# Optimization experiments

Hardware: AMD Instinct MI355X
Metric: run time of the kernel (lower is better)

## Reference

```python
import jax, jax.numpy as jnp
import numpy as np
import math

FIRE_THRESH = 0.85
SQRT_2_OVER_PI = math.sqrt(2.0 / math.pi)

def _gelu(x):
    # tanh-approx GELU, exactly as in the torch module
    return 0.5 * x * (1.0 + jnp.tanh(SQRT_2_OVER_PI * (x + 0.044715 * x * x * x)))

def setup_inputs() -> dict:
    key = jax.random.key(0)
    ks = jax.random.split(key, 8)
    B, T, D, N = 8, 4096, 1024, 512
    x = jax.random.normal(ks[0], (B, T, D), dtype=jnp.float32)
    log_beta = jnp.asarray(math.log(10.0), dtype=jnp.float32)
    log_k_inject = jnp.asarray(math.log(0.1), dtype=jnp.float32)
    # buffer keys are stored L2-normalized in the original module
    raw_keys = jax.random.normal(ks[1], (N, D), dtype=jnp.float32)
    buf_keys = raw_keys / jnp.maximum(jnp.linalg.norm(raw_keys, axis=-1, keepdims=True), 1e-12)
    buf_vals = jax.random.normal(ks[2], (N, D), dtype=jnp.float32)
    global_sum = jax.random.normal(ks[3], (D,), dtype=jnp.float32)
    mask = jnp.ones((N,), dtype=bool)
    hit_count = jax.random.randint(ks[4], (N,), 0, 100, dtype=jnp.int64 if jax.config.jax_enable_x64 else jnp.int32)
    n_global = 300
    return {"x": x, "log_beta": log_beta, "log_k_inject": log_k_inject,
            "buf_keys": buf_keys, "buf_vals": buf_vals, "global_sum": global_sum,
            "mask": mask, "hit_count": hit_count, "n_global": n_global}

def reference(x, log_beta, log_k_inject, buf_keys, buf_vals, global_sum, mask, hit_count, n_global):
    B, T, D = x.shape
    y = _gelu(x)  # [B,T,D]
    # m_curr = mean over all tokens, detached in the original
    m_curr = jax.lax.stop_gradient(jnp.mean(y.reshape(-1, D), axis=0))  # [D]
    beta = jnp.clip(jnp.exp(log_beta), 1.0, 50.0)
    k_inject = jnp.clip(jnp.exp(log_k_inject), 0.001, 2.0)
    # retrieval (no_grad block in torch)
    q = m_curr / jnp.maximum(jnp.linalg.norm(m_curr), 1e-12)  # [D]
    sims = buf_keys @ q                                        # [N]
    logits = jnp.where(mask, beta * sims, -1e9)
    attn = jax.nn.softmax(logits, axis=0)
    retrieved = attn @ buf_vals                                # [D]
    nearest_idx = jnp.argmax(logits)
    sims_plain = jnp.where(mask, sims, -1.0)
    hit = hit_count[nearest_idx] + (sims_plain[nearest_idx] > FIRE_THRESH).astype(hit_count.dtype)
    t = k_inject * jnp.log(hit.astype(x.dtype) + 1.0)
    global_mean = global_sum / max(int(n_global), 1)
    delta = jax.lax.stop_gradient(retrieved - global_mean)     # [D]
    return y + t * delta.reshape(1, 1, D)
```

## Files before the change

### kernel.cpp

```cpp
#include <hip/hip_runtime.h>
#include <math.h>

#define ROWS 32768
#define D    1024
#define DF4  256
#define NKEYS 512

__device__ __forceinline__ float gelu1(float x) {
    float z = 0.7978845608028654f * fmaf(0.044715f * x, x * x, x);
    float e = __expf(2.0f * z);
    return x - x / (e + 1.0f);
}

__global__ __launch_bounds__(256) void k_colsum(const float4* __restrict__ x4,
                                                float4* __restrict__ partial) {
    int t = threadIdx.x;
    int b = blockIdx.x;
    const float4* p = x4 + (size_t)b * 64 * DF4 + t;
    float4 acc = make_float4(0.f, 0.f, 0.f, 0.f);
#pragma unroll 8
    for (int r = 0; r < 64; ++r) {
        float4 v = p[(size_t)r * DF4];
        acc.x += gelu1(v.x);
        acc.y += gelu1(v.y);
        acc.z += gelu1(v.z);
        acc.w += gelu1(v.w);
    }
    partial[b * DF4 + t] = acc;
}

__global__ __launch_bounds__(1024) void k_red1(const float* __restrict__ partial,
                                               float* __restrict__ partial2) {
    int d = threadIdx.x;
    int b = blockIdx.x;
    float s = 0.f;
#pragma unroll
    for (int p = 0; p < 32; ++p) s += partial[(size_t)(b * 32 + p) * D + d];
    partial2[b * D + d] = s;
}

__global__ __launch_bounds__(1024) void k_q(const float* __restrict__ partial2,
                                            float* __restrict__ q) {
    __shared__ float red[1024];
    int d = threadIdx.x;
    float s = 0.f;
#pragma unroll
    for (int p = 0; p < 16; ++p) s += partial2[p * D + d];
    float m = s * (1.0f / 32768.0f);
    red[d] = m * m;
    __syncthreads();
    for (int st = 512; st > 0; st >>= 1) {
        if (d < st) red[d] += red[d + st];
        __syncthreads();
    }
    float inv = 1.0f / fmaxf(sqrtf(red[0]), 1e-12f);
    q[d] = m * inv;
}

__global__ __launch_bounds__(256) void k_sims(const float4* __restrict__ keys4,
                                              const float4* __restrict__ q4,
                                              float* __restrict__ sims) {
    int n = blockIdx.x;
    int t = threadIdx.x;
    float4 k = keys4[(size_t)n * DF4 + t];
    float4 qq = q4[t];
    float v = k.x * qq.x + k.y * qq.y + k.z * qq.z + k.w * qq.w;
#pragma unroll
    for (int off = 32; off > 0; off >>= 1) v += __shfl_down(v, off, 64);
    __shared__ float wsum[4];
    int wave = t >> 6, lane = t & 63;
    if (lane == 0) wsum[wave] = v;
    __syncthreads();
    if (t == 0) sims[n] = wsum[0] + wsum[1] + wsum[2] + wsum[3];
}

__global__ __launch_bounds__(512) void k_softmax(const float* __restrict__ sims,
                                                 const float* __restrict__ log_beta,
                                                 const float* __restrict__ log_k_inject,
                                                 const int* __restrict__ hit_count,
                                                 float* __restrict__ attn,
                                                 float* __restrict__ tval) {
    __shared__ float sval[512];
    __shared__ int   sidx[512];
    __shared__ float ssum[512];
    int n = threadIdx.x;
    float beta = fminf(fmaxf(expf(log_beta[0]), 1.0f), 50.0f);
    float s = sims[n];
    float logit = beta * s;
    sval[n] = logit;
    sidx[n] = n;
    __syncthreads();
    for (int st = 256; st > 0; st >>= 1) {
        if (n < st) {
            float ov = sval[n + st];
            int   oi = sidx[n + st];
            if (ov > sval[n] || (ov == sval[n] && oi < sidx[n])) {
                sval[n] = ov;
                sidx[n] = oi;
            }
        }
        __syncthreads();
    }
    float lmax = sval[0];
    int   nearest = sidx[0];
    float e = expf(logit - lmax);
    ssum[n] = e;
    __syncthreads();
    for (int st = 256; st > 0; st >>= 1) {
        if (n < st) ssum[n] += ssum[n + st];
        __syncthreads();
    }
    attn[n] = e / ssum[0];
    if (n == 0) {
        float sp = sims[nearest];
        int hit = hit_count[nearest] + (sp > 0.85f ? 1 : 0);
        float kinj = fminf(fmaxf(expf(log_k_inject[0]), 0.001f), 2.0f);
        tval[0] = kinj * logf((float)hit + 1.0f);
    }
}

__global__ __launch_bounds__(256) void k_rpart(const float4* __restrict__ vals4,
                                               const float* __restrict__ attn,
                                               float4* __restrict__ rpart) {
    int b = blockIdx.x, t = threadIdx.x;
    float4 acc = make_float4(0.f, 0.f, 0.f, 0.f);
#pragma unroll
    for (int j = 0; j < 16; ++j) {
        int n = b * 16 + j;
        float a = attn[n];
        float4 v = vals4[(size_t)n * DF4 + t];
        acc.x = fmaf(a, v.x, acc.x);
        acc.y = fmaf(a, v.y, acc.y);
        acc.z = fmaf(a, v.z, acc.z);
        acc.w = fmaf(a, v.w, acc.w);
    }
    rpart[b * DF4 + t] = acc;
}

__global__ __launch_bounds__(256) void k_addvec(const float4* __restrict__ rpart,
                                                const float4* __restrict__ gsum4,
                                                const int* __restrict__ ngl,
                                                const float* __restrict__ tval,
                                                float4* __restrict__ addvec) {
    int t = threadIdx.x;
    float4 acc = make_float4(0.f, 0.f, 0.f, 0.f);
#pragma unroll
    for (int b = 0; b < 32; ++b) {
        float4 v = rpart[b * DF4 + t];
        acc.x += v.x; acc.y += v.y; acc.z += v.z; acc.w += v.w;
    }
    int ng = ngl[0];
    float invn = 1.0f / (float)(ng > 1 ? ng : 1);
    float tv = tval[0];
    float4 g = gsum4[t];
    float4 o;
    o.x = tv * (acc.x - g.x * invn);
    o.y = tv * (acc.y - g.y * invn);
    o.z = tv * (acc.z - g.z * invn);
    o.w = tv * (acc.w - g.w * invn);
    addvec[t] = o;
}

__global__ __launch_bounds__(256) void k_out(const float4* __restrict__ x4,
                                             const float4* __restrict__ addvec,
                                             float4* __restrict__ out4) {
    const int NF4 = ROWS * DF4;
    int stride = gridDim.x * 256;
    for (int i = blockIdx.x * 256 + threadIdx.x; i < NF4; i += stride) {
        float4 v = x4[i];
        float4 a = addvec[i & (DF4 - 1)];
        float4 o;
        o.x = gelu1(v.x) + a.x;
        o.y = gelu1(v.y) + a.y;
        o.z = gelu1(v.z) + a.z;
        o.w = gelu1(v.w) + a.w;
        out4[i] = o;
    }
}

extern "C" void kernel_launch(void* const* d_in, const int* in_sizes, int n_in,
                              void* d_out, int out_size, void* d_ws, size_t ws_size,
                              hipStream_t stream) {
    const float* x          = (const float*)d_in[0];
    const float* log_beta   = (const float*)d_in[1];
    const float* log_kinj   = (const float*)d_in[2];
    const float* buf_keys   = (const float*)d_in[3];
    const float* buf_vals   = (const float*)d_in[4];
    const float* global_sum = (const float*)d_in[5];
    const int*   hit_count  = (const int*)d_in[7];
    const int*   n_global   = (const int*)d_in[8];
    float* out = (float*)d_out;

    float* ws = (float*)d_ws;
    float* partial  = ws;
    float* partial2 = partial + 512 * 1024;
    float* q        = partial2 + 16 * 1024;
    float* sims     = q + 1024;
    float* attn     = sims + 512;
    float* tval     = attn + 512;
    float* rpart    = tval + 4;
    float* addvec   = rpart + 32 * 1024;

    k_colsum<<<512, 256, 0, stream>>>((const float4*)x, (float4*)partial);
    k_red1<<<16, 1024, 0, stream>>>(partial, partial2);
    k_q<<<1, 1024, 0, stream>>>(partial2, q);
    k_sims<<<NKEYS, 256, 0, stream>>>((const float4*)buf_keys, (const float4*)q, sims);
    k_softmax<<<1, 512, 0, stream>>>(sims, log_beta, log_kinj, hit_count, attn, tval);
    k_rpart<<<32, 256, 0, stream>>>((const float4*)buf_vals, attn, (float4*)rpart);
    k_addvec<<<1, 256, 0, stream>>>((const float4*)rpart, (const float4*)global_sum,
                                    n_global, tval, (float4*)addvec);
    k_out<<<4096, 256, 0, stream>>>((const float4*)x, (const float4*)addvec, (float4*)out);
}
```

Before: 89.93 us.

## Fuse small reduction kernels via fixed-point atomics and last-block tail work

Drops the separate partial-reduction, norm, softmax and addvec kernels. Column sums and retrieved vectors are now accumulated with 64-bit fixed-point atomics, which keeps the result deterministic, and a last-block-done counter runs the softmax and final add-vector step inside the producer kernels. This cuts the number of launches from eight to five and removes the intermediate partial buffers, at the cost of atomic contention and a fixed-point precision limit. The addvec load in the output kernel is also hoisted out of the loop.

Result: slower. 131.8 us (+46.6%).

```diff
diff --git a/kernel.cpp b/kernel.cpp
--- a/kernel.cpp
+++ b/kernel.cpp
@@ -5,6 +5,14 @@
 #define D    1024
 #define DF4  256
 #define NKEYS 512
+#define CS_BLOCKS 512
+#define CS_ROWS   64
+#define SIMS_BLOCKS 16
+#define RP_BLOCKS 32
+
+#define FP_SCALE 4294967296.0
+#define FP_INV   (1.0/4294967296.0)
+#define MEAN_INV (1.0/(4294967296.0*32768.0))
 
 __device__ __forceinline__ float gelu1(float x) {
     float z = 0.7978845608028654f * fmaf(0.044715f * x, x * x, x);
@@ -12,152 +20,166 @@
     return x - x / (e + 1.0f);
 }
 
+__global__ __launch_bounds__(256) void k_zero(unsigned long long* __restrict__ macc,
+                                              unsigned long long* __restrict__ racc,
+                                              int* __restrict__ counters) {
+    int t = threadIdx.x;
+#pragma unroll
+    for (int j = 0; j < 4; ++j) { macc[t*4+j] = 0ull; racc[t*4+j] = 0ull; }
+    if (t < 4) counters[t] = 0;
+}
+
 __global__ __launch_bounds__(256) void k_colsum(const float4* __restrict__ x4,
-                                                float4* __restrict__ partial) {
-    int t = threadIdx.x;
-    int b = blockIdx.x;
-    const float4* p = x4 + (size_t)b * 64 * DF4 + t;
+                                                unsigned long long* __restrict__ macc) {
+    int t = threadIdx.x, b = blockIdx.x;
+    const float4* p = x4 + (size_t)b * CS_ROWS * DF4 + t;
     float4 acc = make_float4(0.f, 0.f, 0.f, 0.f);
 #pragma unroll 8
-    for (int r = 0; r < 64; ++r) {
+    for (int r = 0; r < CS_ROWS; ++r) {
         float4 v = p[(size_t)r * DF4];
-        acc.x += gelu1(v.x);
-        acc.y += gelu1(v.y);
-        acc.z += gelu1(v.z);
-        acc.w += gelu1(v.w);
-    }
-    partial[b * DF4 + t] = acc;
-}
-
-__global__ __launch_bounds__(1024) void k_red1(const float* __restrict__ partial,
-                                               float* __restrict__ partial2) {
-    int d = threadIdx.x;
-    int b = blockIdx.x;
-    float s = 0.f;
-#pragma unroll
-    for (int p = 0; p < 32; ++p) s += partial[(size_t)(b * 32 + p) * D + d];
-    partial2[b * D + d] = s;
-}
-
-__global__ __launch_bounds__(1024) void k_q(const float* __restrict__ partial2,
-                                            float* __restrict__ q) {
-    __shared__ float red[1024];
-    int d = threadIdx.x;
-    float s = 0.f;
-#pragma unroll
-    for (int p = 0; p < 16; ++p) s += partial2[p * D + d];
-    float m = s * (1.0f / 32768.0f);
-    red[d] = m * m;
-    __syncthreads();
-    for (int st = 512; st > 0; st >>= 1) {
-        if (d < st) red[d] += red[d + st];
-        __syncthreads();
-    }
-    float inv = 1.0f / fmaxf(sqrtf(red[0]), 1e-12f);
-    q[d] = m * inv;
+        acc.x += gelu1(v.x); acc.y += gelu1(v.y);
+        acc.z += gelu1(v.z); acc.w += gelu1(v.w);
+    }
+    atomicAdd(&macc[4*t+0], (unsigned long long)(long long)((double)acc.x * FP_SCALE));
+    atomicAdd(&macc[4*t+1], (unsigned long long)(long long)((double)acc.y * FP_SCALE));
+    atomicAdd(&macc[4*t+2], (unsigned long long)(long long)((double)acc.z * FP_SCALE));
+    atomicAdd(&macc[4*t+3], (unsigned long long)(long long)((double)acc.w * FP_SCALE));
 }
 
 __global__ __launch_bounds__(256) void k_sims(const float4* __restrict__ keys4,
-                                              const float4* __restrict__ q4,
-                                              float* __restrict__ sims) {
-    int n = blockIdx.x;
-    int t = threadIdx.x;
-    float4 k = keys4[(size_t)n * DF4 + t];
-    float4 qq = q4[t];
-    float v = k.x * qq.x + k.y * qq.y + k.z * qq.z + k.w * qq.w;
-#pragma unroll
-    for (int off = 32; off > 0; off >>= 1) v += __shfl_down(v, off, 64);
-    __shared__ float wsum[4];
+                                              const unsigned long long* __restrict__ macc,
+                                              const float* __restrict__ log_beta,
+                                              const float* __restrict__ log_kinj,
+                                              const int* __restrict__ hit_count,
+                                              float* __restrict__ sims,
+                                              float* __restrict__ attn,
+                                              float* __restrict__ tval,
+                                              int* __restrict__ cnt) {
+    int t = threadIdx.x, b = blockIdx.x;
     int wave = t >> 6, lane = t & 63;
-    if (lane == 0) wsum[wave] = v;
-    __syncthreads();
-    if (t == 0) sims[n] = wsum[0] + wsum[1] + wsum[2] + wsum[3];
-}
-
-__global__ __launch_bounds__(512) void k_softmax(const float* __restrict__ sims,
-                                                 const float* __restrict__ log_beta,
-                                                 const float* __restrict__ log_k_inject,
-                                                 const int* __restrict__ hit_count,
-                                                 float* __restrict__ attn,
-                                                 float* __restrict__ tval) {
-    __shared__ float sval[512];
-    __shared__ int   sidx[512];
-    __shared__ float ssum[512];
-    int n = threadIdx.x;
-    float beta = fminf(fmaxf(expf(log_beta[0]), 1.0f), 50.0f);
-    float s = sims[n];
-    float logit = beta * s;
-    sval[n] = logit;
-    sidx[n] = n;
-    __syncthreads();
-    for (int st = 256; st > 0; st >>= 1) {
-        if (n < st) {
-            float ov = sval[n + st];
-            int   oi = sidx[n + st];
-            if (ov > sval[n] || (ov == sval[n] && oi < sidx[n])) {
-                sval[n] = ov;
-                sidx[n] = oi;
-            }
+    float4 mq[4];
+#pragma unroll
+    for (int p = 0; p < 4; ++p) {
+        const unsigned long long* mm = &macc[4*(p*64+lane)];
+        mq[p].x = (float)((double)(long long)mm[0] * MEAN_INV);
+        mq[p].y = (float)((double)(long long)mm[1] * MEAN_INV);
+        mq[p].z = (float)((double)(long long)mm[2] * MEAN_INV);
+        mq[p].w = (float)((double)(long long)mm[3] * MEAN_INV);
+    }
+#pragma unroll
+    for (int j = 0; j < 8; ++j) {
+        int n = b * 32 + wave * 8 + j;
+        const float4* kr = keys4 + (size_t)n * DF4;
+        float s = 0.f;
+#pragma unroll
+        for (int p = 0; p < 4; ++p) {
+            float4 k = kr[p*64 + lane];
+            s += k.x*mq[p].x + k.y*mq[p].y + k.z*mq[p].z + k.w*mq[p].w;
+        }
+#pragma unroll
+        for (int off = 32; off > 0; off >>= 1) s += __shfl_down(s, off, 64);
+        if (lane == 0) sims[n] = s;
+    }
+    __threadfence();
+    __syncthreads();
+    __shared__ int lastFlag;
+    if (t == 0) lastFlag = (atomicAdd(cnt, 1) == SIMS_BLOCKS - 1);
+    __syncthreads();
+    if (!lastFlag) return;
+
+    __shared__ float s_norm2;
+    if (wave == 0) {
+        float ss = 0.f;
+#pragma unroll
+        for (int p = 0; p < 4; ++p)
+            ss += mq[p].x*mq[p].x + mq[p].y*mq[p].y + mq[p].z*mq[p].z + mq[p].w*mq[p].w;
+#pragma unroll
+        for (int off = 32; off > 0; off >>= 1) ss += __shfl_down(ss, off, 64);
+        if (lane == 0) s_norm2 = ss;
+    }
+    __syncthreads();
+    float beta = fminf(fmaxf(__expf(log_beta[0]), 1.0f), 50.0f);
+    float inv_norm = 1.0f / fmaxf(sqrtf(s_norm2), 1e-12f);
+    volatile float* vs = sims;
+    float r0 = vs[t], r1 = vs[t + 256];
+    float l0 = beta * (r0 * inv_norm), l1 = beta * (r1 * inv_norm);
+    __shared__ float mval[256];
+    __shared__ int   midx[256];
+    __shared__ float esum[256];
+    float mv; int mi;
+    if (l1 > l0) { mv = l1; mi = t + 256; } else { mv = l0; mi = t; }
+    mval[t] = mv; midx[t] = mi;
+    __syncthreads();
+    for (int st = 128; st > 0; st >>= 1) {
+        if (t < st) {
+            float ov = mval[t+st]; int oi = midx[t+st];
+            if (ov > mval[t] || (ov == mval[t] && oi < midx[t])) { mval[t] = ov; midx[t] = oi; }
         }
         __syncthreads();
     }
-    float lmax = sval[0];
-    int   nearest = sidx[0];
-    float e = expf(logit - lmax);
-    ssum[n] = e;
-    __syncthreads();
-    for (int st = 256; st > 0; st >>= 1) {
-        if (n < st) ssum[n] += ssum[n + st];
+    float lmax = mval[0];
+    float e0 = __expf(l0 - lmax), e1 = __expf(l1 - lmax);
+    esum[t] = e0 + e1;
+    __syncthreads();
+    for (int st = 128; st > 0; st >>= 1) {
+        if (t < st) esum[t] += esum[t+st];
         __syncthreads();
     }
-    attn[n] = e / ssum[0];
-    if (n == 0) {
-        float sp = sims[nearest];
+    float inv_sum = 1.0f / esum[0];
+    attn[t]       = e0 * inv_sum;
+    attn[t + 256] = e1 * inv_sum;
+    if (t == 0) {
+        int nearest = midx[0];
+        float sp = vs[nearest] * inv_norm;
         int hit = hit_count[nearest] + (sp > 0.85f ? 1 : 0);
-        float kinj = fminf(fmaxf(expf(log_k_inject[0]), 0.001f), 2.0f);
+        float kinj = fminf(fmaxf(__expf(log_kinj[0]), 0.001f), 2.0f);
         tval[0] = kinj * logf((float)hit + 1.0f);
     }
 }
 
 __global__ __launch_bounds__(256) void k_rpart(const float4* __restrict__ vals4,
                                                const float* __restrict__ attn,
-                                               float4* __restrict__ rpart) {
-    int b = blockIdx.x, t = threadIdx.x;
+                                               const float4* __restrict__ gsum4,
+                                               const int* __restrict__ ngl,
+                                               const float* __restrict__ tval,
+                                               unsigned long long* __restrict__ racc,
+                                               int* __restrict__ cnt,
+                                               float4* __restrict__ addvec) {
+    int t = threadIdx.x, b = blockIdx.x;
     float4 acc = make_float4(0.f, 0.f, 0.f, 0.f);
 #pragma unroll
     for (int j = 0; j < 16; ++j) {
         int n = b * 16 + j;
         float a = attn[n];
         float4 v = vals4[(size_t)n * DF4 + t];
-        acc.x = fmaf(a, v.x, acc.x);
-        acc.y = fmaf(a, v.y, acc.y);
-        acc.z = fmaf(a, v.z, acc.z);
-        acc.w = fmaf(a, v.w, acc.w);
-    }
-    rpart[b * DF4 + t] = acc;
-}
-
-__global__ __launch_bounds__(256) void k_addvec(const float4* __restrict__ rpart,
-                                                const float4* __restrict__ gsum4,
-                                                const int* __restrict__ ngl,
-                                                const float* __restrict__ tval,
-                                                float4* __restrict__ addvec) {
-    int t = threadIdx.x;
-    float4 acc = make_float4(0.f, 0.f, 0.f, 0.f);
-#pragma unroll
-    for (int b = 0; b < 32; ++b) {
-        float4 v = rpart[b * DF4 + t];
-        acc.x += v.x; acc.y += v.y; acc.z += v.z; acc.w += v.w;
-    }
+        acc.x = fmaf(a, v.x, acc.x); acc.y = fmaf(a, v.y, acc.y);
+        acc.z = fmaf(a, v.z, acc.z); acc.w = fmaf(a, v.w, acc.w);
+    }
+    atomicAdd(&racc[4*t+0], (unsigned long long)(long long)((double)acc.x * FP_SCALE));
+    atomicAdd(&racc[4*t+1], (unsigned long long)(long long)((double)acc.y * FP_SCALE));
+    atomicAdd(&racc[4*t+2], (unsigned long long)(long long)((double)acc.z * FP_SCALE));
+    atomicAdd(&racc[4*t+3], (unsigned long long)(long long)((double)acc.w * FP_SCALE));
+    __threadfence();
+    __syncthreads();
+    __shared__ int lastFlag;
+    if (t == 0) lastFlag = (atomicAdd(cnt, 1) == RP_BLOCKS - 1);
+    __syncthreads();
+    if (!lastFlag) return;
+
+    volatile unsigned long long* vr = racc;
+    float rx = (float)((double)(long long)vr[4*t+0] * FP_INV);
+    float ry = (float)((double)(long long)vr[4*t+1] * FP_INV);
+    float rz = (float)((double)(long long)vr[4*t+2] * FP_INV);
+    float rw = (float)((double)(long long)vr[4*t+3] * FP_INV);
     int ng = ngl[0];
     float invn = 1.0f / (float)(ng > 1 ? ng : 1);
     float tv = tval[0];
     float4 g = gsum4[t];
     float4 o;
-    o.x = tv * (acc.x - g.x * invn);
-    o.y = tv * (acc.y - g.y * invn);
-    o.z = tv * (acc.z - g.z * invn);
-    o.w = tv * (acc.w - g.w * invn);
+    o.x = tv * (rx - g.x * invn);
+    o.y = tv * (ry - g.y * invn);
+    o.z = tv * (rz - g.z * invn);
+    o.w = tv * (rw - g.w * invn);
     addvec[t] = o;
 }
 
@@ -165,10 +187,11 @@
                                              const float4* __restrict__ addvec,
                                              float4* __restrict__ out4) {
     const int NF4 = ROWS * DF4;
+    int i0 = blockIdx.x * 256 + threadIdx.x;
     int stride = gridDim.x * 256;
-    for (int i = blockIdx.x * 256 + threadIdx.x; i < NF4; i += stride) {
+    float4 a = addvec[i0 & (DF4 - 1)];
+    for (int i = i0; i < NF4; i += stride) {
         float4 v = x4[i];
-        float4 a = addvec[i & (DF4 - 1)];
         float4 o;
         o.x = gelu1(v.x) + a.x;
         o.y = gelu1(v.y) + a.y;
@@ -191,23 +214,21 @@
     const int*   n_global   = (const int*)d_in[8];
     float* out = (float*)d_out;
 
-    float* ws = (float*)d_ws;
-    float* partial  = ws;
-    float* partial2 = partial + 512 * 1024;
-    float* q        = partial2 + 16 * 1024;
-    float* sims     = q + 1024;
+    unsigned long long* macc = (unsigned long long*)d_ws;
+    unsigned long long* racc = macc + 1024;
+    int*   counters = (int*)(racc + 1024);
+    float* sims     = (float*)(counters + 4);
     float* attn     = sims + 512;
     float* tval     = attn + 512;
-    float* rpart    = tval + 4;
-    float* addvec   = rpart + 32 * 1024;
-
-    k_colsum<<<512, 256, 0, stream>>>((const float4*)x, (float4*)partial);
-    k_red1<<<16, 1024, 0, stream>>>(partial, partial2);
-    k_q<<<1, 1024, 0, stream>>>(partial2, q);
-    k_sims<<<NKEYS, 256, 0, stream>>>((const float4*)buf_keys, (const float4*)q, sims);
-    k_softmax<<<1, 512, 0, stream>>>(sims, log_beta, log_kinj, hit_count, attn, tval);
-    k_rpart<<<32, 256, 0, stream>>>((const float4*)buf_vals, attn, (float4*)rpart);
-    k_addvec<<<1, 256, 0, stream>>>((const float4*)rpart, (const float4*)global_sum,
-                                    n_global, tval, (float4*)addvec);
-    k_out<<<4096, 256, 0, stream>>>((const float4*)x, (const float4*)addvec, (float4*)out);
-}
+    float* addvec   = tval + 4;
+
+    k_zero  <<<1, 256, 0, stream>>>(macc, racc, counters);
+    k_colsum<<<CS_BLOCKS, 256, 0, stream>>>((const float4*)x, macc);
+    k_sims  <<<SIMS_BLOCKS, 256, 0, stream>>>((const float4*)buf_keys, macc,
+                                              log_beta, log_kinj, hit_count,
+                                              sims, attn, tval, &counters[0]);
+    k_rpart <<<RP_BLOCKS, 256, 0, stream>>>((const float4*)buf_vals, attn,
+                                            (const float4*)global_sum, n_global, tval,
+                                            racc, &counters[1], (float4*)addvec);
+    k_out   <<<4096, 256, 0, stream>>>((const float4*)x, (const float4*)addvec, (float4*)out);
+}
```
